# Kernel tuning notes

Hardware: AMD Instinct MI355X
Metric: run time of the kernel (lower is better)

The kernel has to match this reference:

```python
import jax, jax.numpy as jnp
import numpy as np

HEADS = 16
DIM_HEAD = 64
EPS_NORM = 1e-12  # torch F.normalize eps


def _layer_norm(x, gamma):
    mu = jnp.mean(x, axis=-1, keepdims=True)
    var = jnp.var(x, axis=-1, keepdims=True)
    return (x - mu) / jnp.sqrt(var + 1e-5) * gamma


def _rms_qk_norm(x, gamma):
    # x: [b, h, n, d]; gamma: [h, 1, d]; F.normalize then * sqrt(d) * gamma
    nrm = jnp.sqrt(jnp.sum(x * x, axis=-1, keepdims=True))
    normed = x / jnp.maximum(nrm, EPS_NORM)
    return normed * (DIM_HEAD ** 0.5) * gamma[None, :, :, :]


def setup_inputs() -> dict:
    key = jax.random.key(0)
    ks = jax.random.split(key, 6)
    b, n, dim = 2, 2048, 1024
    inner = HEADS * DIM_HEAD
    x = jax.random.normal(ks[0], (b, n, dim), dtype=jnp.float32)
    mask = jax.random.randint(ks[1], (b, n), 0, 2) > 0
    mask = mask.at[:, 0].set(True)  # ensure at least one valid key per row
    s = 1.0 / np.sqrt(dim)
    Wq = jax.random.normal(ks[2], (dim, inner), dtype=jnp.float32) * s
    Wkv = jax.random.normal(ks[3], (dim, 2 * inner), dtype=jnp.float32) * s
    Wo = jax.random.normal(ks[4], (inner, dim), dtype=jnp.float32) * (1.0 / np.sqrt(inner))
    gamma_ln = jnp.ones((dim,), jnp.float32)
    gamma_q = jnp.ones((HEADS, 1, DIM_HEAD), jnp.float32)
    gamma_k = jnp.ones((HEADS, 1, DIM_HEAD), jnp.float32)
    return {"x": x, "mask": mask, "gamma_ln": gamma_ln, "gamma_q": gamma_q,
            "gamma_k": gamma_k, "Wq": Wq, "Wkv": Wkv, "Wo": Wo}


def reference(x, mask, gamma_ln, gamma_q, gamma_k, Wq, Wkv, Wo):
    b, n, dim = x.shape
    h, d = HEADS, DIM_HEAD
    xn = _layer_norm(x, gamma_ln)
    q = jnp.einsum('bnc,ce->bne', xn, Wq)
    kv = jnp.einsum('bnc,ce->bne', xn, Wkv)
    k, v = jnp.split(kv, 2, axis=-1)
    # [b, n, h*d] -> [b, h, n, d]
    q = q.reshape(b, n, h, d).transpose(0, 2, 1, 3)
    k = k.reshape(b, n, h, d).transpose(0, 2, 1, 3)
    v = v.reshape(b, n, h, d).transpose(0, 2, 1, 3)
    q = _rms_qk_norm(q, gamma_q)
    k = _rms_qk_norm(k, gamma_k)
    dots = jnp.einsum('bhid,bhjd->bhij', q, k)  # [b, h, n, n]
    neg = -jnp.finfo(dots.dtype).max
    dots = jnp.where(mask[:, None, None, :], dots, neg)
    attn = jax.nn.softmax(dots, axis=-1)
    out = jnp.einsum('bhij,bhjd->bhid', attn, v)
    out = out.transpose(0, 2, 1, 3).reshape(b, n, h * d)
    return jnp.einsum('bne,ec->bnc', out, Wo)
```

## Files before the change

### kernel.cpp

```cpp
#include <hip/hip_runtime.h>

using u16 = unsigned short;
using u32 = unsigned int;

#define B_   2
#define N_   2048
#define DIM_ 1024
#define H_   16
#define D_   64
#define ROWS_ (B_*N_)
#define E3_  3072

typedef __attribute__((ext_vector_type(8))) short short8;
typedef __attribute__((ext_vector_type(4))) short short4v;
typedef __attribute__((ext_vector_type(4))) float f32x4;

__device__ __forceinline__ u16 f2bf(float f) {
  u32 u = __builtin_bit_cast(u32, f);
  u32 r = (u + 0x7FFFu + ((u >> 16) & 1u)) >> 16;
  return (u16)r;
}
__device__ __forceinline__ float bf2f(u16 h) {
  u32 u = ((u32)h) << 16;
  return __builtin_bit_cast(float, u);
}
__device__ __forceinline__ short8 ld8(const u16* p) { return *(const short8*)p; }
__device__ __forceinline__ f32x4 mfma16(short8 a, short8 b, f32x4 c) {
  return __builtin_amdgcn_mfma_f32_16x16x32_bf16(a, b, c, 0, 0, 0);
}
__device__ __forceinline__ f32x4 mfma16k16(short4v a, short4v b, f32x4 c) {
#if !defined(__HIP_DEVICE_COMPILE__)
  (void)a; (void)b;
  return c;
#elif __has_builtin(__builtin_amdgcn_mfma_f32_16x16x16bf16_1k)
  return __builtin_amdgcn_mfma_f32_16x16x16bf16_1k(a, b, c, 0, 0, 0);
#else
  short8 a8 = (short8){a[0], a[1], a[2], a[3], 0, 0, 0, 0};
  short8 b8 = (short8){b[0], b[1], b[2], b[3], 0, 0, 0, 0};
  return __builtin_amdgcn_mfma_f32_16x16x32_bf16(a8, b8, c, 0, 0, 0);
#endif
}
__device__ __forceinline__ void lds16(const u16* g, u16* l) {
  __builtin_amdgcn_global_load_lds(
      (const __attribute__((address_space(1))) void*)g,
      (__attribute__((address_space(3))) void*)l, 16, 0, 0);
}
__device__ __forceinline__ u32 swzb(u32 L) { return L ^ (((L >> 7) & 7) << 4); }

__global__ __launch_bounds__(256) void k_layernorm(const float* __restrict__ x,
                                                   const float* __restrict__ gamma,
                                                   u16* __restrict__ xn) {
  int row = blockIdx.x, tid = threadIdx.x;
  const float4 xv = *(const float4*)(x + (size_t)row * DIM_ + tid * 4);
  float s = xv.x + xv.y + xv.z + xv.w;
  float q = xv.x*xv.x + xv.y*xv.y + xv.z*xv.z + xv.w*xv.w;
  for (int off = 32; off; off >>= 1) { s += __shfl_xor(s, off); q += __shfl_xor(q, off); }
  __shared__ float red[8];
  int wave = tid >> 6, lane = tid & 63;
  if (lane == 0) { red[wave] = s; red[4 + wave] = q; }
  __syncthreads();
  s = red[0] + red[1] + red[2] + red[3];
  q = red[4] + red[5] + red[6] + red[7];
  float mu  = s * (1.0f / DIM_);
  float var = q * (1.0f / DIM_) - mu * mu;
  float inv = rsqrtf(var + 1e-5f);
  const float4 gv = *(const float4*)(gamma + tid * 4);
  ushort4 ov;
  ov.x = f2bf((xv.x - mu) * inv * gv.x);
  ov.y = f2bf((xv.y - mu) * inv * gv.y);
  ov.z = f2bf((xv.z - mu) * inv * gv.z);
  ov.w = f2bf((xv.w - mu) * inv * gv.w);
  *(ushort4*)(xn + (size_t)row * DIM_ + tid * 4) = ov;
}

__global__ __launch_bounds__(256) void k_tcast(const float* __restrict__ in,
                                               u16* __restrict__ out, int ncols) {
  __shared__ float tile[32][33];
  int tx = threadIdx.x, ty = threadIdx.y;
  int col  = blockIdx.x * 32 + tx;
  int row0 = blockIdx.y * 32;
  for (int j = 0; j < 32; j += 8)
    tile[ty + j][tx] = in[(size_t)(row0 + ty + j) * ncols + col];
  __syncthreads();
  int orow = blockIdx.x * 32 + ty;
  int ocol = row0 + tx;
  for (int j = 0; j < 32; j += 8)
    out[(size_t)(orow + j) * DIM_ + ocol] = f2bf(tile[tx][ty + j]);
}

__global__ void k_mask(const int* __restrict__ mraw, float* __restrict__ bias) {
  __shared__ int flag;
  int tid = threadIdx.x;
  if (tid == 0) flag = 0;
  __syncthreads();
  int v = mraw[tid];
  if (v != 0 && v != 1) atomicOr(&flag, 1);
  __syncthreads();
  bool bytemode = (flag != 0);
  const unsigned char* mb = (const unsigned char*)mraw;
  if (tid < 512) {
    int j = blockIdx.x * 512 + tid;
    bool valid = bytemode ? (mb[j] != 0) : (mraw[j] != 0);
    bias[j] = valid ? 0.0f : -1e30f;
  }
}

template <int NF, bool OUT_BF16>
__global__ __launch_bounds__(256) void k_gemm_bt(const u16* __restrict__ A,
                                                 const u16* __restrict__ Bt,
                                                 void* __restrict__ Cv,
                                                 int M, int Ncols, int K) {
  constexpr int BN = NF * 32;
  __shared__ u16 As[128 * 32];
  __shared__ u16 Bs[BN * 32];
  const int tid = threadIdx.x;
  const int wave = tid >> 6, lane = tid & 63;
  const int g = lane >> 4, li = lane & 15;
  const int gx = gridDim.x;
  const int wg = blockIdx.y * gx + blockIdx.x;
  const int per = (gx * gridDim.y) >> 3;
  const int swz = (wg & 7) * per + (wg >> 3);
  const int tm = (swz % gx) * 128, tn = (swz / gx) * BN;
  const int wm = (wave >> 1) * 64, wn = (wave & 1) * (NF * 16);
  const int srow = wave * 16 + (lane >> 2);
  const int scol = (lane & 3) * 8;

  f32x4 acc[4][NF];
#pragma unroll
  for (int i = 0; i < 4; ++i)
#pragma unroll
    for (int j = 0; j < NF; ++j) acc[i][j] = (f32x4){0.f, 0.f, 0.f, 0.f};

  const u16* ag = A  + (size_t)(tm + srow) * K + scol;
  const u16* bg = Bt + (size_t)(tn + srow) * K + scol;

  for (int k0 = 0; k0 < K; k0 += 32) {
    __syncthreads();
#pragma unroll
    for (int p = 0; p < 2; ++p)
      lds16(ag + (size_t)p * 64 * K + k0, As + p * 2048 + wave * 512);
#pragma unroll
    for (int p = 0; p < NF / 2; ++p)
      lds16(bg + (size_t)p * 64 * K + k0, Bs + p * 2048 + wave * 512);
    __syncthreads();
    short8 af[4], bfm[NF];
#pragma unroll
    for (int m = 0; m < 4; ++m) af[m]  = ld8(As + (wm + m * 16 + li) * 32 + g * 8);
#pragma unroll
    for (int n = 0; n < NF; ++n) bfm[n] = ld8(Bs + (wn + n * 16 + li) * 32 + g * 8);
#pragma unroll
    for (int m = 0; m < 4; ++m)
#pragma unroll
      for (int n = 0; n < NF; ++n)
        acc[m][n] = mfma16(af[m], bfm[n], acc[m][n]);
  }
#pragma unroll
  for (int m = 0; m < 4; ++m)
#pragma unroll
    for (int n = 0; n < NF; ++n) {
      int row = tm + wm + m * 16 + g * 4;
      int col = tn + wn + n * 16 + li;
#pragma unroll
      for (int r = 0; r < 4; ++r) {
        float v = acc[m][n][r];
        if (OUT_BF16) ((u16*)Cv)[(size_t)(row + r) * Ncols + col] = f2bf(v);
        else          ((float*)Cv)[(size_t)(row + r) * Ncols + col] = v;
      }
    }
}

__global__ __launch_bounds__(256) void k_rms_qk(const u16* __restrict__ Cq,
                                                const float* __restrict__ gq,
                                                const float* __restrict__ gk,
                                                u16* __restrict__ qo,
                                                u16* __restrict__ ko) {
  int gid = blockIdx.x * 32 + (threadIdx.x >> 3);
  int sub = threadIdx.x & 7;
  int hh  = gid & 31;
  int row = gid >> 5;
  int b = row >> 11, n = row & 2047;
  bool isq = hh < 16;
  int h = hh & 15;
  int col = (isq ? 0 : 1024) + h * 64 + sub * 8;
  short8 v8 = ld8(Cq + (size_t)row * E3_ + col);
  float f[8], ss = 0.f;
#pragma unroll
  for (int j = 0; j < 8; ++j) { f[j] = bf2f((u16)v8[j]); ss += f[j] * f[j]; }
  ss += __shfl_xor(ss, 1);
  ss += __shfl_xor(ss, 2);
  ss += __shfl_xor(ss, 4);
  float scale = 8.0f / fmaxf(sqrtf(ss), 1e-12f);
  const float* gam = (isq ? gq : gk) + h * 64 + sub * 8;
  ushort4 o0, o1;
  o0.x = f2bf(f[0] * scale * gam[0]); o0.y = f2bf(f[1] * scale * gam[1]);
  o0.z = f2bf(f[2] * scale * gam[2]); o0.w = f2bf(f[3] * scale * gam[3]);
  o1.x = f2bf(f[4] * scale * gam[4]); o1.y = f2bf(f[5] * scale * gam[5]);
  o1.z = f2bf(f[6] * scale * gam[6]); o1.w = f2bf(f[7] * scale * gam[7]);
  u16* dst = (isq ? qo : ko) + (((size_t)(b * H_ + h)) * N_ + n) * 64 + sub * 8;
  *(ushort4*)dst = o0;
  *(ushort4*)(dst + 4) = o1;
}

__global__ __launch_bounds__(256) void k_vt(const u16* __restrict__ Cq,
                                            u16* __restrict__ vT) {
  __shared__ float tile[64][65];
  int bh = blockIdx.y;
  int b = bh >> 4, h = bh & 15;
  int n0 = blockIdx.x * 64;
  int tx = threadIdx.x, ty = threadIdx.y;
  for (int i = 0; i < 64; i += 4) {
    int n = n0 + ty + i;
    tile[ty + i][tx] = bf2f(Cq[((size_t)(b * N_ + n)) * E3_ + 2048 + h * 64 + tx]);
  }
  __syncthreads();
  u16* dst = vT + (size_t)bh * 64 * N_;
  for (int i = 0; i < 64; i += 4) {
    int d = ty + i;
    dst[(size_t)d * N_ + n0 + tx] = f2bf(tile[tx][d]);
  }
}

__global__ __launch_bounds__(256, 4) void k_attn(const u16* __restrict__ Q,
                                                 const u16* __restrict__ K,
                                                 const u16* __restrict__ Vt,
                                                 const float* __restrict__ bias,
                                                 u16* __restrict__ Out) {
  __shared__ u16 Ks[2][4096];
  __shared__ u16 Vs[2][4096];
  __shared__ float bias_s[N_];
  int wg = blockIdx.x;
  int xcd = wg & 7, slot = wg >> 3;
  int bh = xcd * 4 + (slot & 3);
  int qb = (slot >> 2) * 64;
  int b = bh >> 4, h = bh & 15;
  int tid = threadIdx.x, wave = tid >> 6, lane = tid & 63;
  int g = lane >> 4, li = lane & 15;
  const u16* Qh = Q  + (size_t)bh * N_ * 64;
  const u16* Kh = K  + (size_t)bh * N_ * 64;
  const u16* Vh = Vt + (size_t)bh * 64 * N_;

  for (int j = tid; j < N_; j += 256) bias_s[j] = bias[b * N_ + j];

  const u32 L0 = tid * 16, L1 = tid * 16 + 4096;
  const u32 kS0 = swzb(L0) >> 1, kS1 = swzb(L1) >> 1;
  const u32 vR0 = L0 >> 7, vR1 = L1 >> 7;
  const u32 vC0 = (swzb(L0) & 127) >> 1, vC1 = (swzb(L1) & 127) >> 1;

  int qr = qb + wave * 16 + li;
  short8 aq0 = ld8(Qh + (size_t)qr * 64 + g * 8);
  short8 aq1 = ld8(Qh + (size_t)qr * 64 + 32 + g * 8);

  f32x4 oT[4];
#pragma unroll
  for (int dc = 0; dc < 4; ++dc) oT[dc] = (f32x4){0.f, 0.f, 0.f, 0.f};
  float m = -3e38f, l = 0.f;

  const int fsw  = 8 * (g ^ (li & 7));
  const int fsw2 = fsw ^ 32;
  const int vbl = li * 64 + (g & 1) * 4;
  int vsw[4];
#pragma unroll
  for (int c = 0; c < 4; ++c)
    vsw[c] = (((2 * c + (g >> 1)) ^ (li & 7)) << 3);

  lds16(Kh + kS0, &Ks[0][0] + (L0 >> 1));
  lds16(Kh + kS1, &Ks[0][0] + (L1 >> 1));
  lds16(Vh + (size_t)vR0 * N_ + vC0, &Vs[0][0] + (L0 >> 1));
  lds16(Vh + (size_t)vR1 * N_ + vC1, &Vs[0][0] + (L1 >> 1));
  __syncthreads();

  for (int kt = 0; kt < 32; ++kt) {
    int cur = kt & 1;
    int kbase = kt * 64;
    if (kt < 31) {
      int nxt = cur ^ 1;
      int nb = kbase + 64;
      lds16(Kh + (size_t)nb * 64 + kS0, &Ks[nxt][0] + (L0 >> 1));
      lds16(Kh + (size_t)nb * 64 + kS1, &Ks[nxt][0] + (L1 >> 1));
      lds16(Vh + (size_t)vR0 * N_ + nb + vC0, &Vs[nxt][0] + (L0 >> 1));
      lds16(Vh + (size_t)vR1 * N_ + nb + vC1, &Vs[nxt][0] + (L1 >> 1));
    }
    const u16* Kb = &Ks[cur][0];
    const u16* Vb = &Vs[cur][0];
    f32x4 st[4];
    __builtin_amdgcn_s_setprio(1);
#pragma unroll
    for (int c = 0; c < 4; ++c) {
      int rb = (c * 16 + li) * 64;
      short8 kf0 = ld8(Kb + rb + fsw);
      short8 kf1 = ld8(Kb + rb + fsw2);
      float4 bb = *(const float4*)&bias_s[kbase + c * 16 + g * 4];
      f32x4 z = (f32x4){bb.x, bb.y, bb.z, bb.w};
      z = mfma16(kf0, aq0, z);
      st[c] = mfma16(kf1, aq1, z);
    }
    __builtin_amdgcn_s_setprio(0);
    short4v vf16[4][4];
#pragma unroll
    for (int dc = 0; dc < 4; ++dc)
#pragma unroll
      for (int c = 0; c < 4; ++c)
        vf16[dc][c] = *(const short4v*)(Vb + dc * 1024 + vbl + vsw[c]);
    float cm[4];
#pragma unroll
    for (int c = 0; c < 4; ++c)
      cm[c] = fmaxf(fmaxf(st[c][0], st[c][1]), fmaxf(st[c][2], st[c][3]));
    float tmax = fmaxf(fmaxf(cm[0], cm[1]), fmaxf(cm[2], cm[3]));
    tmax = fmaxf(tmax, __shfl_xor(tmax, 16));
    tmax = fmaxf(tmax, __shfl_xor(tmax, 32));
    float mn = fmaxf(m, tmax);
    float sc = __expf(m - mn);
    m = mn;
    float pv[4][4], cs[4];
#pragma unroll
    for (int c = 0; c < 4; ++c) {
#pragma unroll
      for (int r = 0; r < 4; ++r) pv[c][r] = __expf(st[c][r] - mn);
      cs[c] = (pv[c][0] + pv[c][1]) + (pv[c][2] + pv[c][3]);
    }
    float rs = (cs[0] + cs[1]) + (cs[2] + cs[3]);
    rs += __shfl_xor(rs, 16);
    rs += __shfl_xor(rs, 32);
    l = l * sc + rs;
#pragma unroll
    for (int dc = 0; dc < 4; ++dc) oT[dc] *= sc;
    union { u32 u2[2]; short4v s4; } pb[4];
#pragma unroll
    for (int c = 0; c < 4; ++c) {
      asm("v_cvt_pk_bf16_f32 %0, %1, %2" : "=v"(pb[c].u2[0]) : "v"(pv[c][0]), "v"(pv[c][1]));
      asm("v_cvt_pk_bf16_f32 %0, %1, %2" : "=v"(pb[c].u2[1]) : "v"(pv[c][2]), "v"(pv[c][3]));
    }
    __builtin_amdgcn_s_setprio(1);
#pragma unroll
    for (int dc = 0; dc < 4; ++dc)
#pragma unroll
      for (int c = 0; c < 4; ++c)
        oT[dc] = mfma16k16(vf16[dc][c], pb[c].s4, oT[dc]);
    __builtin_amdgcn_s_setprio(0);
    __syncthreads();
  }

  float inv = 1.0f / l;
#pragma unroll
  for (int dc = 0; dc < 4; ++dc) {
    ushort4 ov;
    ov.x = f2bf(oT[dc][0] * inv);
    ov.y = f2bf(oT[dc][1] * inv);
    ov.z = f2bf(oT[dc][2] * inv);
    ov.w = f2bf(oT[dc][3] * inv);
    *(ushort4*)&Out[((size_t)(b * N_ + qr)) * DIM_ + h * 64 + dc * 16 + g * 4] = ov;
  }
}

extern "C" void kernel_launch(void* const* d_in, const int* in_sizes, int n_in,
                              void* d_out, int out_size, void* d_ws, size_t ws_size,
                              hipStream_t stream) {
  const float* x    = (const float*)d_in[0];
  const int*   mask = (const int*)d_in[1];
  const float* g_ln = (const float*)d_in[2];
  const float* g_q  = (const float*)d_in[3];
  const float* g_k  = (const float*)d_in[4];
  const float* Wq   = (const float*)d_in[5];
  const float* Wkv  = (const float*)d_in[6];
  const float* Wo   = (const float*)d_in[7];
  float* out = (float*)d_out;

  char* ws = (char*)d_ws;
  u16*   xn   = (u16*)(ws);
  u16*   Wt   = (u16*)(ws + 8388608);
  u16*   Wot  = (u16*)(ws + 14680064);
  float* bias = (float*)(ws + 16777216);
  u16*   Cq   = (u16*)(ws + 16793600);
  u16*   qb   = (u16*)(ws + 41959424);
  u16*   kb   = (u16*)(ws + 41959424 + 8388608);
  u16*   vT   = (u16*)(ws + 41959424 + 2*8388608);
  u16*   ao   = (u16*)(ws + 41959424 + 3*8388608);

  k_layernorm<<<ROWS_, 256, 0, stream>>>(x, g_ln, xn);
  dim3 tcb(32, 8);
  k_tcast<<<dim3(32, 32), tcb, 0, stream>>>(Wq,  Wt,               1024);
  k_tcast<<<dim3(64, 32), tcb, 0, stream>>>(Wkv, Wt + 1024 * 1024, 2048);
  k_tcast<<<dim3(32, 32), tcb, 0, stream>>>(Wo,  Wot,              1024);
  k_mask<<<8, 1024, 0, stream>>>(mask, bias);
  k_gemm_bt<4, true><<<dim3(32, 24), 256, 0, stream>>>(xn, Wt, Cq, ROWS_, E3_, DIM_);
  k_rms_qk<<<4096, 256, 0, stream>>>(Cq, g_q, g_k, qb, kb);
  k_vt<<<dim3(32, 32), dim3(64, 4), 0, stream>>>(Cq, vT);
  k_attn<<<1024, 256, 0, stream>>>(qb, kb, vT, bias, ao);
  k_gemm_bt<2, false><<<dim3(32, 16), 256, 0, stream>>>(ao, Wot, out, ROWS_, DIM_, DIM_);
}
```

Before: 161.1 us.

## Process two query tiles per wave in attention and merge weight transpose launches

The attention kernel now runs 128 threads (2 waves) per block, and each wave handles 32 query rows as two 16-row sub-tiles. The K and V fragments read from LDS are reused across both sub-tiles, which halves LDS reads per MFMA but roughly doubles accumulator and score registers per wave. Each thread now issues four async LDS loads per tile instead of two. The three weight transpose-cast launches are also merged into one kernel that picks its source by block index, saving launch overhead.

```diff
diff --git a/kernel.cpp b/kernel.cpp
--- a/kernel.cpp
+++ b/kernel.cpp
@@ -73,16 +73,24 @@
   *(ushort4*)(xn + (size_t)row * DIM_ + tid * 4) = ov;
 }
 
-__global__ __launch_bounds__(256) void k_tcast(const float* __restrict__ in,
-                                               u16* __restrict__ out, int ncols) {
+__global__ __launch_bounds__(256) void k_tcast_all(const float* __restrict__ Wq,
+                                                   const float* __restrict__ Wkv,
+                                                   const float* __restrict__ Wo,
+                                                   u16* __restrict__ Wt,
+                                                   u16* __restrict__ Wot) {
   __shared__ float tile[32][33];
+  int bx = blockIdx.x;
+  const float* in; u16* out; int ncols, cb;
+  if (bx < 32)      { in = Wq;  out = Wt;               ncols = 1024; cb = bx; }
+  else if (bx < 96) { in = Wkv; out = Wt + 1024 * 1024; ncols = 2048; cb = bx - 32; }
+  else              { in = Wo;  out = Wot;              ncols = 1024; cb = bx - 96; }
   int tx = threadIdx.x, ty = threadIdx.y;
-  int col  = blockIdx.x * 32 + tx;
+  int col  = cb * 32 + tx;
   int row0 = blockIdx.y * 32;
   for (int j = 0; j < 32; j += 8)
     tile[ty + j][tx] = in[(size_t)(row0 + ty + j) * ncols + col];
   __syncthreads();
-  int orow = blockIdx.x * 32 + ty;
+  int orow = cb * 32 + ty;
   int ocol = row0 + tx;
   for (int j = 0; j < 32; j += 8)
     out[(size_t)(orow + j) * DIM_ + ocol] = f2bf(tile[tx][ty + j]);
@@ -220,7 +228,7 @@
   }
 }
 
-__global__ __launch_bounds__(256, 4) void k_attn(const u16* __restrict__ Q,
+__global__ __launch_bounds__(128, 2) void k_attn(const u16* __restrict__ Q,
                                                  const u16* __restrict__ K,
                                                  const u16* __restrict__ Vt,
                                                  const float* __restrict__ bias,
@@ -239,21 +247,31 @@
   const u16* Kh = K  + (size_t)bh * N_ * 64;
   const u16* Vh = Vt + (size_t)bh * 64 * N_;
 
-  for (int j = tid; j < N_; j += 256) bias_s[j] = bias[b * N_ + j];
-
-  const u32 L0 = tid * 16, L1 = tid * 16 + 4096;
-  const u32 kS0 = swzb(L0) >> 1, kS1 = swzb(L1) >> 1;
-  const u32 vR0 = L0 >> 7, vR1 = L1 >> 7;
-  const u32 vC0 = (swzb(L0) & 127) >> 1, vC1 = (swzb(L1) & 127) >> 1;
-
-  int qr = qb + wave * 16 + li;
-  short8 aq0 = ld8(Qh + (size_t)qr * 64 + g * 8);
-  short8 aq1 = ld8(Qh + (size_t)qr * 64 + 32 + g * 8);
-
-  f32x4 oT[4];
-#pragma unroll
-  for (int dc = 0; dc < 4; ++dc) oT[dc] = (f32x4){0.f, 0.f, 0.f, 0.f};
-  float m = -3e38f, l = 0.f;
+  for (int j = tid; j < N_; j += 128) bias_s[j] = bias[b * N_ + j];
+
+  u32 Ls[4], kS[4], vR[4], vC[4];
+#pragma unroll
+  for (int s = 0; s < 4; ++s) {
+    Ls[s] = tid * 16 + s * 2048;
+    kS[s] = swzb(Ls[s]) >> 1;
+    vR[s] = Ls[s] >> 7;
+    vC[s] = (swzb(Ls[s]) & 127) >> 1;
+  }
+
+  int qr0 = qb + wave * 32 + li;
+  int qr1 = qr0 + 16;
+  short8 aqA0 = ld8(Qh + (size_t)qr0 * 64 + g * 8);
+  short8 aqA1 = ld8(Qh + (size_t)qr0 * 64 + 32 + g * 8);
+  short8 aqB0 = ld8(Qh + (size_t)qr1 * 64 + g * 8);
+  short8 aqB1 = ld8(Qh + (size_t)qr1 * 64 + 32 + g * 8);
+
+  f32x4 oTA[4], oTB[4];
+#pragma unroll
+  for (int dc = 0; dc < 4; ++dc) {
+    oTA[dc] = (f32x4){0.f, 0.f, 0.f, 0.f};
+    oTB[dc] = (f32x4){0.f, 0.f, 0.f, 0.f};
+  }
+  float mA = -3e38f, lA = 0.f, mB = -3e38f, lB = 0.f;
 
   const int fsw  = 8 * (g ^ (li & 7));
   const int fsw2 = fsw ^ 32;
@@ -263,10 +281,11 @@
   for (int c = 0; c < 4; ++c)
     vsw[c] = (((2 * c + (g >> 1)) ^ (li & 7)) << 3);
 
-  lds16(Kh + kS0, &Ks[0][0] + (L0 >> 1));
-  lds16(Kh + kS1, &Ks[0][0] + (L1 >> 1));
-  lds16(Vh + (size_t)vR0 * N_ + vC0, &Vs[0][0] + (L0 >> 1));
-  lds16(Vh + (size_t)vR1 * N_ + vC1, &Vs[0][0] + (L1 >> 1));
+#pragma unroll
+  for (int s = 0; s < 4; ++s) {
+    lds16(Kh + kS[s], &Ks[0][0] + (Ls[s] >> 1));
+    lds16(Vh + (size_t)vR[s] * N_ + vC[s], &Vs[0][0] + (Ls[s] >> 1));
+  }
   __syncthreads();
 
   for (int kt = 0; kt < 32; ++kt) {
@@ -275,14 +294,15 @@
     if (kt < 31) {
       int nxt = cur ^ 1;
       int nb = kbase + 64;
-      lds16(Kh + (size_t)nb * 64 + kS0, &Ks[nxt][0] + (L0 >> 1));
-      lds16(Kh + (size_t)nb * 64 + kS1, &Ks[nxt][0] + (L1 >> 1));
-      lds16(Vh + (size_t)vR0 * N_ + nb + vC0, &Vs[nxt][0] + (L0 >> 1));
-      lds16(Vh + (size_t)vR1 * N_ + nb + vC1, &Vs[nxt][0] + (L1 >> 1));
+#pragma unroll
+      for (int s = 0; s < 4; ++s) {
+        lds16(Kh + (size_t)nb * 64 + kS[s], &Ks[nxt][0] + (Ls[s] >> 1));
+        lds16(Vh + (size_t)vR[s] * N_ + nb + vC[s], &Vs[nxt][0] + (Ls[s] >> 1));
+      }
     }
     const u16* Kb = &Ks[cur][0];
     const u16* Vb = &Vs[cur][0];
-    f32x4 st[4];
+    f32x4 stA[4], stB[4];
     __builtin_amdgcn_s_setprio(1);
 #pragma unroll
     for (int c = 0; c < 4; ++c) {
@@ -291,8 +311,8 @@
       short8 kf1 = ld8(Kb + rb + fsw2);
       float4 bb = *(const float4*)&bias_s[kbase + c * 16 + g * 4];
       f32x4 z = (f32x4){bb.x, bb.y, bb.z, bb.w};
-      z = mfma16(kf0, aq0, z);
-      st[c] = mfma16(kf1, aq1, z);
+      stA[c] = mfma16(kf1, aqA1, mfma16(kf0, aqA0, z));
+      stB[c] = mfma16(kf1, aqB1, mfma16(kf0, aqB0, z));
     }
     __builtin_amdgcn_s_setprio(0);
     short4v vf16[4][4];
@@ -301,54 +321,82 @@
 #pragma unroll
       for (int c = 0; c < 4; ++c)
         vf16[dc][c] = *(const short4v*)(Vb + dc * 1024 + vbl + vsw[c]);
-    float cm[4];
+    float cmA[4];
 #pragma unroll
     for (int c = 0; c < 4; ++c)
-      cm[c] = fmaxf(fmaxf(st[c][0], st[c][1]), fmaxf(st[c][2], st[c][3]));
-    float tmax = fmaxf(fmaxf(cm[0], cm[1]), fmaxf(cm[2], cm[3]));
-    tmax = fmaxf(tmax, __shfl_xor(tmax, 16));
-    tmax = fmaxf(tmax, __shfl_xor(tmax, 32));
-    float mn = fmaxf(m, tmax);
-    float sc = __expf(m - mn);
-    m = mn;
-    float pv[4][4], cs[4];
+      cmA[c] = fmaxf(fmaxf(stA[c][0], stA[c][1]), fmaxf(stA[c][2], stA[c][3]));
+    float tmaxA = fmaxf(fmaxf(cmA[0], cmA[1]), fmaxf(cmA[2], cmA[3]));
+    tmaxA = fmaxf(tmaxA, __shfl_xor(tmaxA, 16));
+    tmaxA = fmaxf(tmaxA, __shfl_xor(tmaxA, 32));
+    float mnA = fmaxf(mA, tmaxA);
+    float scA = __expf(mA - mnA);
+    mA = mnA;
+    float pvA[4][4], csA[4];
 #pragma unroll
     for (int c = 0; c < 4; ++c) {
 #pragma unroll
-      for (int r = 0; r < 4; ++r) pv[c][r] = __expf(st[c][r] - mn);
-      cs[c] = (pv[c][0] + pv[c][1]) + (pv[c][2] + pv[c][3]);
-    }
-    float rs = (cs[0] + cs[1]) + (cs[2] + cs[3]);
-    rs += __shfl_xor(rs, 16);
-    rs += __shfl_xor(rs, 32);
-    l = l * sc + rs;
-#pragma unroll
-    for (int dc = 0; dc < 4; ++dc) oT[dc] *= sc;
-    union { u32 u2[2]; short4v s4; } pb[4];
+      for (int r = 0; r < 4; ++r) pvA[c][r] = __expf(stA[c][r] - mnA);
+      csA[c] = (pvA[c][0] + pvA[c][1]) + (pvA[c][2] + pvA[c][3]);
+    }
+    float rsA = (csA[0] + csA[1]) + (csA[2] + csA[3]);
+    rsA += __shfl_xor(rsA, 16);
+    rsA += __shfl_xor(rsA, 32);
+    lA = lA * scA + rsA;
+#pragma unroll
+    for (int dc = 0; dc < 4; ++dc) oTA[dc] *= scA;
+    float cmB[4];
+#pragma unroll
+    for (int c = 0; c < 4; ++c)
+      cmB[c] = fmaxf(fmaxf(stB[c][0], stB[c][1]), fmaxf(stB[c][2], stB[c][3]));
+    float tmaxB = fmaxf(fmaxf(cmB[0], cmB[1]), fmaxf(cmB[2], cmB[3]));
+    tmaxB = fmaxf(tmaxB, __shfl_xor(tmaxB, 16));
+    tmaxB = fmaxf(tmaxB, __shfl_xor(tmaxB, 32));
+    float mnB = fmaxf(mB, tmaxB);
+    float scB = __expf(mB - mnB);
+    mB = mnB;
+    float pvB[4][4], csB[4];
 #pragma unroll
     for (int c = 0; c < 4; ++c) {
-      asm("v_cvt_pk_bf16_f32 %0, %1, %2" : "=v"(pb[c].u2[0]) : "v"(pv[c][0]), "v"(pv[c][1]));
-      asm("v_cvt_pk_bf16_f32 %0, %1, %2" : "=v"(pb[c].u2[1]) : "v"(pv[c][2]), "v"(pv[c][3]));
+#pragma unroll
+      for (int r = 0; r < 4; ++r) pvB[c][r] = __expf(stB[c][r] - mnB);
+      csB[c] = (pvB[c][0] + pvB[c][1]) + (pvB[c][2] + pvB[c][3]);
+    }
+    float rsB = (csB[0] + csB[1]) + (csB[2] + csB[3]);
+    rsB += __shfl_xor(rsB, 16);
+    rsB += __shfl_xor(rsB, 32);
+    lB = lB * scB + rsB;
+#pragma unroll
+    for (int dc = 0; dc < 4; ++dc) oTB[dc] *= scB;
+    union { u32 u2[2]; short4v s4; } pbA[4], pbB[4];
+#pragma unroll
+    for (int c = 0; c < 4; ++c) {
+      asm("v_cvt_pk_bf16_f32 %0, %1, %2" : "=v"(pbA[c].u2[0]) : "v"(pvA[c][0]), "v"(pvA[c][1]));
+      asm("v_cvt_pk_bf16_f32 %0, %1, %2" : "=v"(pbA[c].u2[1]) : "v"(pvA[c][2]), "v"(pvA[c][3]));
+      asm("v_cvt_pk_bf16_f32 %0, %1, %2" : "=v"(pbB[c].u2[0]) : "v"(pvB[c][0]), "v"(pvB[c][1]));
+      asm("v_cvt_pk_bf16_f32 %0, %1, %2" : "=v"(pbB[c].u2[1]) : "v"(pvB[c][2]), "v"(pvB[c][3]));
     }
     __builtin_amdgcn_s_setprio(1);
 #pragma unroll
     for (int dc = 0; dc < 4; ++dc)
 #pragma unroll
-      for (int c = 0; c < 4; ++c)
-        oT[dc] = mfma16k16(vf16[dc][c], pb[c].s4, oT[dc]);
+      for (int c = 0; c < 4; ++c) {
+        oTA[dc] = mfma16k16(vf16[dc][c], pbA[c].s4, oTA[dc]);
+        oTB[dc] = mfma16k16(vf16[dc][c], pbB[c].s4, oTB[dc]);
+      }
     __builtin_amdgcn_s_setprio(0);
     __syncthreads();
   }
 
-  float inv = 1.0f / l;
+  float invA = 1.0f / lA, invB = 1.0f / lB;
 #pragma unroll
   for (int dc = 0; dc < 4; ++dc) {
-    ushort4 ov;
-    ov.x = f2bf(oT[dc][0] * inv);
-    ov.y = f2bf(oT[dc][1] * inv);
-    ov.z = f2bf(oT[dc][2] * inv);
-    ov.w = f2bf(oT[dc][3] * inv);
-    *(ushort4*)&Out[((size_t)(b * N_ + qr)) * DIM_ + h * 64 + dc * 16 + g * 4] = ov;
+    ushort4 ovA, ovB;
+    ovA.x = f2bf(oTA[dc][0] * invA); ovA.y = f2bf(oTA[dc][1] * invA);
+    ovA.z = f2bf(oTA[dc][2] * invA); ovA.w = f2bf(oTA[dc][3] * invA);
+    ovB.x = f2bf(oTB[dc][0] * invB); ovB.y = f2bf(oTB[dc][1] * invB);
+    ovB.z = f2bf(oTB[dc][2] * invB); ovB.w = f2bf(oTB[dc][3] * invB);
+    *(ushort4*)&Out[((size_t)(b * N_ + qr0)) * DIM_ + h * 64 + dc * 16 + g * 4] = ovA;
+    *(ushort4*)&Out[((size_t)(b * N_ + qr1)) * DIM_ + h * 64 + dc * 16 + g * 4] = ovB;
   }
 }
 
@@ -377,14 +425,11 @@
   u16*   ao   = (u16*)(ws + 41959424 + 3*8388608);
 
   k_layernorm<<<ROWS_, 256, 0, stream>>>(x, g_ln, xn);
-  dim3 tcb(32, 8);
-  k_tcast<<<dim3(32, 32), tcb, 0, stream>>>(Wq,  Wt,               1024);
-  k_tcast<<<dim3(64, 32), tcb, 0, stream>>>(Wkv, Wt + 1024 * 1024, 2048);
-  k_tcast<<<dim3(32, 32), tcb, 0, stream>>>(Wo,  Wot,              1024);
+  k_tcast_all<<<dim3(128, 32), dim3(32, 8), 0, stream>>>(Wq, Wkv, Wo, Wt, Wot);
   k_mask<<<8, 1024, 0, stream>>>(mask, bias);
   k_gemm_bt<4, true><<<dim3(32, 24), 256, 0, stream>>>(xn, Wt, Cq, ROWS_, E3_, DIM_);
   k_rms_qk<<<4096, 256, 0, stream>>>(Cq, g_q, g_k, qb, kb);
   k_vt<<<dim3(32, 32), dim3(64, 4), 0, stream>>>(Cq, vT);
-  k_attn<<<1024, 256, 0, stream>>>(qb, kb, vT, bias, ao);
+  k_attn<<<1024, 128, 0, stream>>>(qb, kb, vT, bias, ao);
   k_gemm_bt<2, false><<<dim3(32, 16), 256, 0, stream>>>(ao, Wot, out, ROWS_, DIM_, DIM_);
 }
```

After: 161.0 us. Within noise of the previous version (-0.0%).
